# Kernel tuning notes

Measured on AMD Instinct MI355X. Metric: run time of the kernel, lower is better.

The kernel has to match this reference:

```python
import jax, jax.numpy as jnp
import numpy as np

B, T, C, H = 8, 2048, 1024, 64

def setup_inputs() -> dict:
    key = jax.random.key(0)
    k1, k2, k3, k4 = jax.random.split(key, 4)
    x = jax.random.normal(k1, (B, T, C), dtype=jnp.float32)
    sw = 1.0 / np.sqrt(C)  # Linear-like init scale
    Wq = jax.random.normal(k2, (C, H), dtype=jnp.float32) * sw
    Wk = jax.random.normal(k3, (C, H), dtype=jnp.float32) * sw
    Wv = jax.random.normal(k4, (C, H), dtype=jnp.float32) * sw
    return {"x": x, "Wq": Wq, "Wk": Wk, "Wv": Wv}

def reference(x, Wq, Wk, Wv):
    # Single-head causal self-attention (eval mode: dropout is identity).
    # Quantized GEMMs (QLinear / qmatmul) are represented by exact fp32 math.
    Bx, Tx, Cx = x.shape
    q = jnp.einsum('btc,ch->bth', x, Wq)          # [B,T,H]
    k = jnp.einsum('btc,ch->bth', x, Wk)          # [B,T,H]
    v = jnp.einsum('btc,ch->bth', x, Wv)          # [B,T,H]
    scale = k.shape[-1] ** -0.5
    wei = jnp.einsum('bth,bsh->bts', q, k) * scale  # [B,T,T]
    causal = jnp.tril(jnp.ones((Tx, Tx), dtype=bool))
    wei = jnp.where(causal, wei, -jnp.inf)
    wei = jax.nn.softmax(wei, axis=-1)
    out = jnp.einsum('bts,bsh->bth', wei, v)      # [B,T,H]
    return out
```

## Files before the change

### kernel.cpp

```cpp
#include <hip/hip_runtime.h>
#include <math.h>

#define Bz 8
#define Tz 2048
#define Cz 1024
#define Hz 64
#define BT (Bz*Tz)

typedef __attribute__((ext_vector_type(8))) short bf16x8;
typedef __attribute__((ext_vector_type(4))) float f32x4;
typedef __attribute__((ext_vector_type(4))) unsigned short us4;

#define PSTRIDE 4160

__device__ __forceinline__ unsigned short f2bf(float f) {
    union { float f; unsigned u; } v; v.f = f;
    unsigned r = v.u + 0x7fffu + ((v.u >> 16) & 1u);
    return (unsigned short)(r >> 16);
}

__device__ __forceinline__ bf16x8 pack8(const float* s) {
    bf16x8 r;
#pragma unroll
    for (int j = 0; j < 8; j++) r[j] = (short)f2bf(s[j]);
    return r;
}

__device__ __forceinline__ unsigned cvt_pk_bf16(float lo, float hi) {
    unsigned r;
    asm volatile("v_cvt_pk_bf16_f32 %0, %1, %2" : "=v"(r) : "v"(lo), "v"(hi));
    return r;
}

__device__ __forceinline__ bf16x8 cvt8(float4 a, float4 b) {
    union { unsigned u[4]; bf16x8 v; } r;
    r.u[0] = cvt_pk_bf16(a.x, a.y);
    r.u[1] = cvt_pk_bf16(a.z, a.w);
    r.u[2] = cvt_pk_bf16(b.x, b.y);
    r.u[3] = cvt_pk_bf16(b.z, b.w);
    return r.v;
}

__device__ __forceinline__ void gload16(const void* g, void* l) {
    __builtin_amdgcn_global_load_lds(
        (const __attribute__((address_space(1))) void*)g,
        (__attribute__((address_space(3))) void*)l, 16, 0, 0);
}

__global__ __launch_bounds__(256)
void wprep_kernel(const float* __restrict__ Wq, const float* __restrict__ Wk,
                  const float* __restrict__ Wv, unsigned short* __restrict__ Wti)
{
    __shared__ float T[64][65];
    const int mat = blockIdx.x >> 4;
    const int kt  = blockIdx.x & 15;
    const int k0  = kt * 64;
    const float* W = (mat == 0) ? Wq : (mat == 1) ? Wk : Wv;
    const int t  = threadIdx.x;
    const int rr = t >> 2;
    const int c4 = (t & 3) * 16;
#pragma unroll
    for (int j = 0; j < 4; j++) {
        float4 w4 = *(const float4*)&W[(size_t)(k0 + rr) * Hz + c4 + j * 4];
        T[c4 + j*4 + 0][rr] = w4.x;
        T[c4 + j*4 + 1][rr] = w4.y;
        T[c4 + j*4 + 2][rr] = w4.z;
        T[c4 + j*4 + 3][rr] = w4.w;
    }
    __syncthreads();
    const int nn  = t >> 2;
    const int sl0 = (t & 3) * 2;
    const int n   = mat * 64 + nn;
    float tmp[16];
#pragma unroll
    for (int j = 0; j < 16; j++) tmp[j] = T[nn][sl0 * 8 + j];
    unsigned short* base = &Wti[(size_t)kt * 12288 + n * 64];
    *(bf16x8*)&base[((sl0    ) ^ (n & 7)) * 8] = pack8(tmp);
    *(bf16x8*)&base[((sl0 + 1) ^ (n & 7)) * 8] = pack8(tmp + 8);
}

__global__ __launch_bounds__(256, 3)
void qkv_mfma_kernel(const float* __restrict__ x, const unsigned short* __restrict__ Wti,
                     unsigned short* __restrict__ qg, unsigned short* __restrict__ kg,
                     unsigned short* __restrict__ vT)
{
    __shared__ __align__(16) unsigned short ws[2][192 * 64];

    const int t    = threadIdx.x;
    const int M0   = blockIdx.x * 32;
    const int ln   = t & 15;
    const int g    = (t & 63) >> 4;
    const int g4   = g * 4;
    const int w    = t >> 6;
    const int wr   = w & 1;
    const int wc   = w >> 1;
    const int lane = t & 63;
    const float SCq = 0.18033688011112042f;

    f32x4 acc[6];
#pragma unroll
    for (int i = 0; i < 6; i++) acc[i] = (f32x4){0.f, 0.f, 0.f, 0.f};

    const float* xrow = &x[(size_t)(M0 + wr * 16 + ln) * Cz + g * 8];

    auto issueW = [&](int buf, int kt) {
#pragma unroll
        for (int j = 0; j < 6; j++) {
            const int jj = w * 6 + j;
            gload16(&Wti[(size_t)kt * 12288 + jj * 512 + lane * 8],
                    &ws[buf][jj * 512]);
        }
    };

    float4 xf[4], xfn[4];
    auto loadX = [&](int kt, float4* d) {
        const float* p = xrow + kt * 64;
        d[0] = *(const float4*)(p);
        d[1] = *(const float4*)(p + 4);
        d[2] = *(const float4*)(p + 32);
        d[3] = *(const float4*)(p + 36);
    };

    issueW(0, 0);
    loadX(0, xf);
    __syncthreads();
    int cur = 0;

    for (int kt = 0; kt < 16; kt++) {
        if (kt < 15) { issueW(cur ^ 1, kt + 1); loadX(kt + 1, xfn); }

        bf16x8 af[2];
        af[0] = cvt8(xf[0], xf[1]);
        af[1] = cvt8(xf[2], xf[3]);

        __builtin_amdgcn_s_setprio(1);
#pragma unroll
        for (int ct = 0; ct < 6; ct++) {
            const int nn = wc * 96 + ct * 16 + ln;
#pragma unroll
            for (int kc = 0; kc < 2; kc++) {
                bf16x8 bf = *(const bf16x8*)&ws[cur][nn * 64 + ((kc*4 + g) ^ (nn & 7)) * 8];
                acc[ct] = __builtin_amdgcn_mfma_f32_16x16x32_bf16(af[kc], bf, acc[ct], 0, 0, 0);
            }
        }
        __builtin_amdgcn_s_setprio(0);
        __syncthreads();
#pragma unroll
        for (int i = 0; i < 4; i++) xf[i] = xfn[i];
        cur ^= 1;
    }

#pragma unroll
    for (int ct = 0; ct < 6; ct++) {
        const int col0 = wc * 96 + ct * 16;
        const int mat  = col0 >> 6;
        const int cl   = (col0 & 63) + ln;
        const int m0   = M0 + wr * 16 + g4;
        if (mat == 0) {
#pragma unroll
            for (int i = 0; i < 4; i++)
                qg[(size_t)(m0 + i) * Hz + cl] = f2bf(acc[ct][i] * SCq);
        } else if (mat == 1) {
#pragma unroll
            for (int i = 0; i < 4; i++)
                kg[(size_t)(m0 + i) * Hz + cl] = f2bf(acc[ct][i]);
        } else {
            const int b = m0 >> 11, tt = m0 & 2047;
            us4 pk;
#pragma unroll
            for (int i = 0; i < 4; i++) pk[i] = f2bf(acc[ct][i]);
            *(us4*)&vT[((size_t)b * Hz + cl) * Tz + tt] = pk;
        }
    }
}

template<int S>
__global__ __launch_bounds__(256, 4)
void attn_mfma_kernel(const unsigned short* __restrict__ qg,
                      const unsigned short* __restrict__ kg,
                      const unsigned short* __restrict__ vT,
                      float* __restrict__ pbase)
{
    __shared__ __align__(16) unsigned short Ks [2][64 * 64];
    __shared__ __align__(16) unsigned short Vts[2][64 * 64];
    __shared__ __align__(16) unsigned short Ps [4 * 16 * 64];

    const int bid = blockIdx.x;
    const int b   = bid & 7;
    const int r0  = bid >> 3;
    const int c   = r0 % S;
    const int qt  = 31 - (r0 / S);
    if (c > qt) return;
    const int q0  = qt * 64;

    const int t  = threadIdx.x;
    const int ln = t & 15;
    const int g  = (t & 63) >> 4;
    const int g4 = g * 4;
    const int w  = t >> 6;
    const int l6 = t & 63;

    const unsigned short* qb = qg + (size_t)b * Tz * Hz;
    const unsigned short* kb = kg + (size_t)b * Tz * Hz;
    const unsigned short* vb = vT + (size_t)b * Hz * Tz;

    const int rl  = l6 >> 3;
    const int swz = ((l6 & 7) ^ rl) * 8;
    auto issue_tile = [&](int buf, int s0) {
#pragma unroll
        for (int qq = 0; qq < 2; qq++) {
            const int row = w*16 + qq*8 + rl;
            gload16(&kb[(size_t)(s0 + row) * Hz + swz],
                    &Ks[buf][(w*16 + qq*8) * 64]);
            gload16(&vb[(size_t)row * Tz + s0 + swz],
                    &Vts[buf][(w*16 + qq*8) * 64]);
        }
    };

    issue_tile(0, c * 64);

    bf16x8 qf[2];
    {
        const int qrow = q0 + w*16 + ln;
        qf[0] = *(const bf16x8*)&qb[(size_t)qrow * Hz + g*8];
        qf[1] = *(const bf16x8*)&qb[(size_t)qrow * Hz + 32 + g*8];
    }

    f32x4 accO[4];
#pragma unroll
    for (int i = 0; i < 4; i++) accO[i] = (f32x4){0.f, 0.f, 0.f, 0.f};
    float lrow = 0.f;
    unsigned short* Pw = &Ps[w * 1024];
    const int pwbase = ln*64 + (g & 1) * 4;
    const int pslotx = (g >> 1);

    __syncthreads();
    int cur = 0;

    for (int s = c; s <= qt; s += S) {
        if (s + S <= qt) issue_tile(cur ^ 1, (s + S) * 64);

        const unsigned short* Kc = &Ks[cur][0];
        const unsigned short* Vc = &Vts[cur][0];

        f32x4 accS[4];
        __builtin_amdgcn_s_setprio(1);
#pragma unroll
        for (int t4 = 0; t4 < 4; t4++) {
            accS[t4] = (f32x4){0.f, 0.f, 0.f, 0.f};
#pragma unroll
            for (int kc = 0; kc < 2; kc++) {
                const int n = t4*16 + ln;
                bf16x8 kf = *(const bf16x8*)&Kc[n*64 + ((kc*4 + g) ^ (n & 7)) * 8];
                accS[t4] = __builtin_amdgcn_mfma_f32_16x16x32_bf16(kf, qf[kc], accS[t4], 0, 0, 0);
            }
        }
        __builtin_amdgcn_s_setprio(0);

        const bool diag = (s == qt);
#pragma unroll
        for (int t4 = 0; t4 < 4; t4++) {
            float pv[4];
#pragma unroll
            for (int i = 0; i < 4; i++) {
                float sv = accS[t4][i];
                if (diag && (t4*16 + g4 + i > w*16 + ln)) sv = -1e30f;
                const float p = exp2f(sv);
                lrow += p;
                pv[i] = p;
            }
            uint2 pk2;
            pk2.x = cvt_pk_bf16(pv[0], pv[1]);
            pk2.y = cvt_pk_bf16(pv[2], pv[3]);
            *(uint2*)&Pw[pwbase + ((t4*2 + pslotx) ^ (ln & 7)) * 8] = pk2;
        }

        __builtin_amdgcn_s_setprio(1);
#pragma unroll
        for (int kc = 0; kc < 2; kc++) {
            bf16x8 pa = *(const bf16x8*)&Pw[ln*64 + ((kc*4 + g) ^ (ln & 7)) * 8];
#pragma unroll
            for (int ht = 0; ht < 4; ht++) {
                const int vr2 = ht*16 + ln;
                bf16x8 vf = *(const bf16x8*)&Vc[vr2*64 + ((kc*4 + g) ^ (vr2 & 7)) * 8];
                accO[ht] = __builtin_amdgcn_mfma_f32_16x16x32_bf16(pa, vf, accO[ht], 0, 0, 0);
            }
        }
        __builtin_amdgcn_s_setprio(0);

        __syncthreads();
        cur ^= 1;
    }

    lrow += __shfl_xor(lrow, 16);
    lrow += __shfl_xor(lrow, 32);

    float* Op = pbase + (size_t)((b * 32 + qt) * S + c) * PSTRIDE;
#pragma unroll
    for (int ht = 0; ht < 4; ht++)
#pragma unroll
        for (int i = 0; i < 4; i++)
            Op[(size_t)(w*16 + g4 + i) * 64 + ht*16 + ln] = accO[ht][i];
    if (g == 0)
        Op[4096 + w*16 + ln] = lrow;
}

template<int S>
__global__ __launch_bounds__(256)
void combine_kernel(const float* __restrict__ pbase, float* __restrict__ out)
{
    const int bid = blockIdx.x;
    const int b   = bid & 7;
    const int qt  = 31 - (bid >> 3);
    const int t   = threadIdx.x;
    const int r   = t >> 2;
    const int cg  = t & 3;

    const int nch = (qt + 1 < S) ? (qt + 1) : S;
    const float* P0 = pbase + (size_t)(b * 32 + qt) * S * PSTRIDE;

    float denom = 0.f;
    float4 o[4];
#pragma unroll
    for (int j = 0; j < 4; j++) o[j] = make_float4(0.f, 0.f, 0.f, 0.f);
    for (int cc = 0; cc < nch; cc++) {
        const float* Pc = P0 + (size_t)cc * PSTRIDE;
        denom += Pc[4096 + r];
#pragma unroll
        for (int j = 0; j < 4; j++) {
            float4 v4 = *(const float4*)&Pc[(size_t)r * 64 + cg * 16 + j * 4];
            o[j].x += v4.x; o[j].y += v4.y; o[j].z += v4.z; o[j].w += v4.w;
        }
    }
    const float inv = 1.f / denom;
    float* ob = out + ((size_t)b * Tz + qt * 64 + r) * Hz + cg * 16;
#pragma unroll
    for (int j = 0; j < 4; j++)
        *(float4*)&ob[j * 4] = make_float4(o[j].x * inv, o[j].y * inv,
                                           o[j].z * inv, o[j].w * inv);
}

extern "C" void kernel_launch(void* const* d_in, const int* in_sizes, int n_in,
                              void* d_out, int out_size, void* d_ws, size_t ws_size,
                              hipStream_t stream) {
    const float* x  = (const float*)d_in[0];
    const float* Wq = (const float*)d_in[1];
    const float* Wk = (const float*)d_in[2];
    const float* Wv = (const float*)d_in[3];

    unsigned short* Wti = (unsigned short*)d_ws;
    unsigned short* qg  = Wti + 196608;
    unsigned short* kg  = qg + (size_t)BT * Hz;
    unsigned short* vT  = kg + (size_t)BT * Hz;
    const size_t baseShorts = 196608 + 3 * (size_t)BT * Hz;
    float* pbase = (float*)((char*)d_ws + baseShorts * 2);
    float* out = (float*)d_out;

    wprep_kernel<<<48, 256, 0, stream>>>(Wq, Wk, Wv, Wti);
    qkv_mfma_kernel<<<BT / 32, 256, 0, stream>>>(x, Wti, qg, kg, vT);

    const size_t base = baseShorts * 2;
    const size_t per  = (size_t)8 * 32 * PSTRIDE * 4;
    if (ws_size >= base + 4 * per) {
        attn_mfma_kernel<4><<<8 * 32 * 4, 256, 0, stream>>>(qg, kg, vT, pbase);
        combine_kernel<4><<<256, 256, 0, stream>>>(pbase, out);
    } else {
        attn_mfma_kernel<1><<<8 * 32 * 1, 256, 0, stream>>>(qg, kg, vT, pbase);
        combine_kernel<1><<<256, 256, 0, stream>>>(pbase, out);
    }
}
```

Measured before the change: 53.11 us.

## Pre-permute weights into MFMA fragment order and load directly to registers

The weight prep kernel now writes bf16 weights already laid out in per-lane MFMA B-fragment order. The QKV projection kernel then loads those fragments straight from global memory into registers, which removes the LDS staging buffers, the async copies and the per-iteration __syncthreads. It software-pipelines with two register sets, wA and wB, alternating across k-tiles, and drops the occupancy hint from launch_bounds. The cost is higher register pressure from 24 bf16x8 fragments, plus redundant global reads of the weights, since waves sharing a column half each load the same data.

```diff
diff --git a/kernel.cpp b/kernel.cpp
--- a/kernel.cpp
+++ b/kernel.cpp
@@ -68,86 +68,90 @@
         T[c4 + j*4 + 3][rr] = w4.w;
     }
     __syncthreads();
-    const int nn  = t >> 2;
-    const int sl0 = (t & 3) * 2;
-    const int n   = mat * 64 + nn;
-    float tmp[16];
-#pragma unroll
-    for (int j = 0; j < 16; j++) tmp[j] = T[nn][sl0 * 8 + j];
-    unsigned short* base = &Wti[(size_t)kt * 12288 + n * 64];
-    *(bf16x8*)&base[((sl0    ) ^ (n & 7)) * 8] = pack8(tmp);
-    *(bf16x8*)&base[((sl0 + 1) ^ (n & 7)) * 8] = pack8(tmp + 8);
-}
-
-__global__ __launch_bounds__(256, 3)
+#pragma unroll
+    for (int h = 0; h < 2; h++) {
+        const int idx = h * 256 + t;
+        const int nn  = idx & 63;
+        const int kg  = idx >> 6;
+        const int kc  = kg >> 2;
+        const int gg  = kg & 3;
+        const int ng  = mat * 64 + nn;
+        const int wcc = (ng >= 96) ? 1 : 0;
+        const int rem = ng - wcc * 96;
+        const int ctt = rem >> 4;
+        const int lnn = rem & 15;
+        float tmp[8];
+#pragma unroll
+        for (int j = 0; j < 8; j++) tmp[j] = T[nn][kc*32 + gg*8 + j];
+        const size_t off = (size_t)kt*12288 + wcc*6144 + (ctt*2 + kc)*512
+                         + (gg*16 + lnn)*8;
+        *(bf16x8*)&Wti[off] = pack8(tmp);
+    }
+}
+
+__global__ __launch_bounds__(256)
 void qkv_mfma_kernel(const float* __restrict__ x, const unsigned short* __restrict__ Wti,
                      unsigned short* __restrict__ qg, unsigned short* __restrict__ kg,
                      unsigned short* __restrict__ vT)
 {
-    __shared__ __align__(16) unsigned short ws[2][192 * 64];
-
-    const int t    = threadIdx.x;
-    const int M0   = blockIdx.x * 32;
-    const int ln   = t & 15;
-    const int g    = (t & 63) >> 4;
-    const int g4   = g * 4;
-    const int w    = t >> 6;
-    const int wr   = w & 1;
-    const int wc   = w >> 1;
-    const int lane = t & 63;
+    const int t  = threadIdx.x;
+    const int M0 = blockIdx.x * 32;
+    const int ln = t & 15;
+    const int g  = (t & 63) >> 4;
+    const int g4 = g * 4;
+    const int w  = t >> 6;
+    const int wr = w & 1;
+    const int wc = w >> 1;
+    const int l6 = t & 63;
     const float SCq = 0.18033688011112042f;
 
     f32x4 acc[6];
 #pragma unroll
     for (int i = 0; i < 6; i++) acc[i] = (f32x4){0.f, 0.f, 0.f, 0.f};
 
-    const float* xrow = &x[(size_t)(M0 + wr * 16 + ln) * Cz + g * 8];
-
-    auto issueW = [&](int buf, int kt) {
-#pragma unroll
-        for (int j = 0; j < 6; j++) {
-            const int jj = w * 6 + j;
-            gload16(&Wti[(size_t)kt * 12288 + jj * 512 + lane * 8],
-                    &ws[buf][jj * 512]);
-        }
+    const float* xrow = &x[(size_t)(M0 + wr*16 + ln) * Cz + g*8];
+    const unsigned short* wbase = Wti + wc*6144 + l6*8;
+
+    auto loadW = [&](int kt, bf16x8* wf) {
+#pragma unroll
+        for (int i = 0; i < 12; i++)
+            wf[i] = *(const bf16x8*)&wbase[(size_t)kt*12288 + i*512];
     };
-
-    float4 xf[4], xfn[4];
     auto loadX = [&](int kt, float4* d) {
-        const float* p = xrow + kt * 64;
+        const float* p = xrow + kt*64;
         d[0] = *(const float4*)(p);
         d[1] = *(const float4*)(p + 4);
         d[2] = *(const float4*)(p + 32);
         d[3] = *(const float4*)(p + 36);
     };
 
-    issueW(0, 0);
-    loadX(0, xf);
-    __syncthreads();
-    int cur = 0;
-
-    for (int kt = 0; kt < 16; kt++) {
-        if (kt < 15) { issueW(cur ^ 1, kt + 1); loadX(kt + 1, xfn); }
-
-        bf16x8 af[2];
-        af[0] = cvt8(xf[0], xf[1]);
-        af[1] = cvt8(xf[2], xf[3]);
-
-        __builtin_amdgcn_s_setprio(1);
-#pragma unroll
-        for (int ct = 0; ct < 6; ct++) {
-            const int nn = wc * 96 + ct * 16 + ln;
-#pragma unroll
-            for (int kc = 0; kc < 2; kc++) {
-                bf16x8 bf = *(const bf16x8*)&ws[cur][nn * 64 + ((kc*4 + g) ^ (nn & 7)) * 8];
-                acc[ct] = __builtin_amdgcn_mfma_f32_16x16x32_bf16(af[kc], bf, acc[ct], 0, 0, 0);
-            }
-        }
-        __builtin_amdgcn_s_setprio(0);
-        __syncthreads();
-#pragma unroll
-        for (int i = 0; i < 4; i++) xf[i] = xfn[i];
-        cur ^= 1;
+    float4 x0[4], x1[4];
+    bf16x8 wA[12], wB[12];
+    loadX(0, x0); loadW(0, wA);
+    loadX(1, x1);
+
+    for (int kt = 0; kt < 16; kt += 2) {
+        if (kt + 1 < 16) loadW(kt + 1, wB);
+        {
+            bf16x8 af0 = cvt8(x0[0], x0[1]);
+            bf16x8 af1 = cvt8(x0[2], x0[3]);
+#pragma unroll
+            for (int ct = 0; ct < 6; ct++) {
+                acc[ct] = __builtin_amdgcn_mfma_f32_16x16x32_bf16(af0, wA[ct*2+0], acc[ct], 0, 0, 0);
+                acc[ct] = __builtin_amdgcn_mfma_f32_16x16x32_bf16(af1, wA[ct*2+1], acc[ct], 0, 0, 0);
+            }
+        }
+        if (kt + 2 < 16) { loadX(kt + 2, x0); loadW(kt + 2, wA); }
+        {
+            bf16x8 af0 = cvt8(x1[0], x1[1]);
+            bf16x8 af1 = cvt8(x1[2], x1[3]);
+#pragma unroll
+            for (int ct = 0; ct < 6; ct++) {
+                acc[ct] = __builtin_amdgcn_mfma_f32_16x16x32_bf16(af0, wB[ct*2+0], acc[ct], 0, 0, 0);
+                acc[ct] = __builtin_amdgcn_mfma_f32_16x16x32_bf16(af1, wB[ct*2+1], acc[ct], 0, 0, 0);
+            }
+        }
+        if (kt + 3 < 16) loadX(kt + 3, x1);
     }
 
 #pragma unroll
```

Measured after the change: 58.90 us. +10.9%, slower.

## Restructure QKV projection into explicit two-stage pipeline with manual vmcnt waits

Applied to the files above, without the earlier changes.

Rewrites the QKV GEMM main loop as an unrolled two-buffer pipeline. Two k-tiles of W and x are kept in flight, and explicit s_waitcnt vmcnt(10) waits with sched_barrier fences replace the compiler-managed syncthreads. Launch bounds are also raised from 3 to 4 blocks per SM to increase occupancy. The aim is to overlap global loads with MFMA compute more deeply. The risks are register pressure from the tighter occupancy bound and correctness hazards from hand-counted vmcnt values.

```diff
diff --git a/kernel.cpp b/kernel.cpp
--- a/kernel.cpp
+++ b/kernel.cpp
@@ -79,7 +79,7 @@
     *(bf16x8*)&base[((sl0 + 1) ^ (n & 7)) * 8] = pack8(tmp + 8);
 }
 
-__global__ __launch_bounds__(256, 3)
+__global__ __launch_bounds__(256, 4)
 void qkv_mfma_kernel(const float* __restrict__ x, const unsigned short* __restrict__ Wti,
                      unsigned short* __restrict__ qg, unsigned short* __restrict__ kg,
                      unsigned short* __restrict__ vT)
@@ -103,7 +103,7 @@
 
     const float* xrow = &x[(size_t)(M0 + wr * 16 + ln) * Cz + g * 8];
 
-    auto issueW = [&](int buf, int kt) {
+    auto gloadW = [&](int buf, int kt) {
 #pragma unroll
         for (int j = 0; j < 6; j++) {
             const int jj = w * 6 + j;
@@ -111,9 +111,7 @@
                     &ws[buf][jj * 512]);
         }
     };
-
-    float4 xf[4], xfn[4];
-    auto loadX = [&](int kt, float4* d) {
+    auto loadx = [&](int kt, float4* d) {
         const float* p = xrow + kt * 64;
         d[0] = *(const float4*)(p);
         d[1] = *(const float4*)(p + 4);
@@ -121,33 +119,56 @@
         d[3] = *(const float4*)(p + 36);
     };
 
-    issueW(0, 0);
-    loadX(0, xf);
-    __syncthreads();
-    int cur = 0;
-
-    for (int kt = 0; kt < 16; kt++) {
-        if (kt < 15) { issueW(cur ^ 1, kt + 1); loadX(kt + 1, xfn); }
-
+    float4 xA[4], xB[4];
+
+    auto compute = [&](int buf, const float4* xr) {
         bf16x8 af[2];
-        af[0] = cvt8(xf[0], xf[1]);
-        af[1] = cvt8(xf[2], xf[3]);
-
+        af[0] = cvt8(xr[0], xr[1]);
+        af[1] = cvt8(xr[2], xr[3]);
         __builtin_amdgcn_s_setprio(1);
 #pragma unroll
         for (int ct = 0; ct < 6; ct++) {
             const int nn = wc * 96 + ct * 16 + ln;
 #pragma unroll
             for (int kc = 0; kc < 2; kc++) {
-                bf16x8 bf = *(const bf16x8*)&ws[cur][nn * 64 + ((kc*4 + g) ^ (nn & 7)) * 8];
+                bf16x8 bf = *(const bf16x8*)&ws[buf][nn * 64 + ((kc*4 + g) ^ (nn & 7)) * 8];
                 acc[ct] = __builtin_amdgcn_mfma_f32_16x16x32_bf16(af[kc], bf, acc[ct], 0, 0, 0);
             }
         }
         __builtin_amdgcn_s_setprio(0);
-        __syncthreads();
-#pragma unroll
-        for (int i = 0; i < 4; i++) xf[i] = xfn[i];
-        cur ^= 1;
+    };
+
+    gloadW(0, 0); loadx(0, xA);
+    gloadW(1, 1); loadx(1, xB);
+    asm volatile("s_waitcnt vmcnt(10)" ::: "memory");
+    __builtin_amdgcn_sched_barrier(0);
+    __builtin_amdgcn_s_barrier();
+
+    for (int kt = 0; kt < 16; kt += 2) {
+        compute(0, xA);
+        __builtin_amdgcn_sched_barrier(0);
+        __builtin_amdgcn_s_barrier();
+        if (kt + 2 < 16) {
+            gloadW(0, kt + 2); loadx(kt + 2, xA);
+            asm volatile("s_waitcnt vmcnt(10)" ::: "memory");
+        } else {
+            asm volatile("s_waitcnt vmcnt(0)" ::: "memory");
+        }
+        __builtin_amdgcn_sched_barrier(0);
+        __builtin_amdgcn_s_barrier();
+
+        compute(1, xB);
+        if (kt + 1 == 15) break;
+        __builtin_amdgcn_sched_barrier(0);
+        __builtin_amdgcn_s_barrier();
+        if (kt + 3 < 16) {
+            gloadW(1, kt + 3); loadx(kt + 3, xB);
+            asm volatile("s_waitcnt vmcnt(10)" ::: "memory");
+        } else {
+            asm volatile("s_waitcnt vmcnt(0)" ::: "memory");
+        }
+        __builtin_amdgcn_sched_barrier(0);
+        __builtin_amdgcn_s_barrier();
     }
 
 #pragma unroll
```

Result: slower. 55.13 us (+3.8%).

## Restructure QKV projection: one matrix per block, full weight slab in LDS

Applied to the files above, without the earlier changes.

The QKV projection kernel now assigns each 512-thread block a 128-row tile and a single output matrix (Q, K or V). The block loads that matrix's full bf16 weight slab (1024x64) into LDS once up front, replacing per-k-step double-buffered weight loads and a barrier on every iteration. X rows are prefetched three k-steps ahead in registers, and the k loop runs fully unrolled with a single barrier. This removes the per-iteration synchronisation and weight reloads. In exchange each row of x is read three times, once per matrix, LDS use per block grows to 128 KB, and the grid shrinks to 384 blocks.

```diff
diff --git a/kernel.cpp b/kernel.cpp
--- a/kernel.cpp
+++ b/kernel.cpp
@@ -79,97 +79,97 @@
     *(bf16x8*)&base[((sl0 + 1) ^ (n & 7)) * 8] = pack8(tmp + 8);
 }
 
-__global__ __launch_bounds__(256, 3)
+__global__ __launch_bounds__(512, 2)
 void qkv_mfma_kernel(const float* __restrict__ x, const unsigned short* __restrict__ Wti,
                      unsigned short* __restrict__ qg, unsigned short* __restrict__ kg,
                      unsigned short* __restrict__ vT)
 {
-    __shared__ __align__(16) unsigned short ws[2][192 * 64];
-
-    const int t    = threadIdx.x;
-    const int M0   = blockIdx.x * 32;
+    __shared__ __align__(16) unsigned short wsAll[16 * 4096];
+
+    const int t     = threadIdx.x;
+    const int bid   = blockIdx.x;
+    const int low   = bid & 7;
+    const int k8    = bid >> 3;
+    const int mat   = k8 % 3;
+    const int mtile = (k8 / 3) * 8 + low;
+    const int M0    = mtile * 128;
+
     const int ln   = t & 15;
     const int g    = (t & 63) >> 4;
     const int g4   = g * 4;
     const int w    = t >> 6;
-    const int wr   = w & 1;
-    const int wc   = w >> 1;
     const int lane = t & 63;
     const float SCq = 0.18033688011112042f;
 
-    f32x4 acc[6];
-#pragma unroll
-    for (int i = 0; i < 6; i++) acc[i] = (f32x4){0.f, 0.f, 0.f, 0.f};
-
-    const float* xrow = &x[(size_t)(M0 + wr * 16 + ln) * Cz + g * 8];
-
-    auto issueW = [&](int buf, int kt) {
-#pragma unroll
-        for (int j = 0; j < 6; j++) {
-            const int jj = w * 6 + j;
-            gload16(&Wti[(size_t)kt * 12288 + jj * 512 + lane * 8],
-                    &ws[buf][jj * 512]);
-        }
-    };
-
-    float4 xf[4], xfn[4];
-    auto loadX = [&](int kt, float4* d) {
+    f32x4 acc[4];
+#pragma unroll
+    for (int i = 0; i < 4; i++) acc[i] = (f32x4){0.f, 0.f, 0.f, 0.f};
+
+#pragma unroll
+    for (int j = 0; j < 16; j++) {
+        const int f  = w * 16 + j;
+        const int kt = f >> 3, rr = f & 7;
+        gload16(&Wti[(size_t)kt * 12288 + (size_t)(mat * 8 + rr) * 512 + lane * 8],
+                &wsAll[f * 512]);
+    }
+    __builtin_amdgcn_sched_barrier(0);
+
+    const float* xrow = &x[(size_t)(M0 + w * 16 + ln) * Cz + g * 8];
+    float4 xp[3][4];
+    auto loadx = [&](int kt, float4* d) {
         const float* p = xrow + kt * 64;
         d[0] = *(const float4*)(p);
         d[1] = *(const float4*)(p + 4);
         d[2] = *(const float4*)(p + 32);
         d[3] = *(const float4*)(p + 36);
     };
-
-    issueW(0, 0);
-    loadX(0, xf);
-    __syncthreads();
-    int cur = 0;
-
+    loadx(0, xp[0]); loadx(1, xp[1]); loadx(2, xp[2]);
+
+    asm volatile("s_waitcnt vmcnt(12)" ::: "memory");
+    __builtin_amdgcn_sched_barrier(0);
+    __builtin_amdgcn_s_barrier();
+    __builtin_amdgcn_sched_barrier(0);
+
+#pragma unroll 16
     for (int kt = 0; kt < 16; kt++) {
-        if (kt < 15) { issueW(cur ^ 1, kt + 1); loadX(kt + 1, xfn); }
-
         bf16x8 af[2];
-        af[0] = cvt8(xf[0], xf[1]);
-        af[1] = cvt8(xf[2], xf[3]);
-
-        __builtin_amdgcn_s_setprio(1);
-#pragma unroll
-        for (int ct = 0; ct < 6; ct++) {
-            const int nn = wc * 96 + ct * 16 + ln;
+        af[0] = cvt8(xp[kt % 3][0], xp[kt % 3][1]);
+        af[1] = cvt8(xp[kt % 3][2], xp[kt % 3][3]);
+        const unsigned short* wk = &wsAll[kt * 4096];
+#pragma unroll
+        for (int ct = 0; ct < 4; ct++) {
+            const int h = ct * 16 + ln;
 #pragma unroll
             for (int kc = 0; kc < 2; kc++) {
-                bf16x8 bf = *(const bf16x8*)&ws[cur][nn * 64 + ((kc*4 + g) ^ (nn & 7)) * 8];
+                bf16x8 bf = *(const bf16x8*)&wk[h * 64 + ((kc*4 + g) ^ (h & 7)) * 8];
                 acc[ct] = __builtin_amdgcn_mfma_f32_16x16x32_bf16(af[kc], bf, acc[ct], 0, 0, 0);
             }
         }
-        __builtin_amdgcn_s_setprio(0);
-        __syncthreads();
-#pragma unroll
-        for (int i = 0; i < 4; i++) xf[i] = xfn[i];
-        cur ^= 1;
-    }
-
-#pragma unroll
-    for (int ct = 0; ct < 6; ct++) {
-        const int col0 = wc * 96 + ct * 16;
-        const int mat  = col0 >> 6;
-        const int cl   = (col0 & 63) + ln;
-        const int m0   = M0 + wr * 16 + g4;
-        if (mat == 0) {
+        if (kt + 3 < 16) loadx(kt + 3, xp[kt % 3]);
+    }
+
+    const int m0 = M0 + w * 16 + g4;
+    if (mat == 0) {
+#pragma unroll
+        for (int ct = 0; ct < 4; ct++)
 #pragma unroll
             for (int i = 0; i < 4; i++)
-                qg[(size_t)(m0 + i) * Hz + cl] = f2bf(acc[ct][i] * SCq);
-        } else if (mat == 1) {
+                qg[(size_t)(m0 + i) * Hz + ct * 16 + ln] = f2bf(acc[ct][i] * SCq);
+    } else if (mat == 1) {
+#pragma unroll
+        for (int ct = 0; ct < 4; ct++)
 #pragma unroll
             for (int i = 0; i < 4; i++)
-                kg[(size_t)(m0 + i) * Hz + cl] = f2bf(acc[ct][i]);
-        } else {
-            const int b = m0 >> 11, tt = m0 & 2047;
+                kg[(size_t)(m0 + i) * Hz + ct * 16 + ln] = f2bf(acc[ct][i]);
+    } else {
+        const int b = m0 >> 11, tt = m0 & 2047;
+#pragma unroll
+        for (int ct = 0; ct < 4; ct++) {
+            const int h = ct * 16 + ln;
             us4 pk;
 #pragma unroll
             for (int i = 0; i < 4; i++) pk[i] = f2bf(acc[ct][i]);
-            *(us4*)&vT[((size_t)b * Hz + cl) * Tz + tt] = pk;
+            *(us4*)&vT[((size_t)b * Hz + h) * Tz + tt] = pk;
         }
     }
 }
@@ -357,7 +357,7 @@
     float* out = (float*)d_out;
 
     wprep_kernel<<<48, 256, 0, stream>>>(Wq, Wk, Wv, Wti);
-    qkv_mfma_kernel<<<BT / 32, 256, 0, stream>>>(x, Wti, qg, kg, vT);
+    qkv_mfma_kernel<<<384, 512, 0, stream>>>(x, Wti, qg, kg, vT);
 
     const size_t base = baseShorts * 2;
     const size_t per  = (size_t)8 * 32 * PSTRIDE * 4;
```

Measured after the change: 62.84 us. 18.3% more time.
